# Kernel optimization log

Hardware: AMD Instinct MI355X
Metric: run time of the kernel (lower is better)

## Reference

```python
import jax, jax.numpy as jnp
import numpy as np
from jax import lax

THRESH = 0.6      # pnet score threshold (threshold[0])
IOU_THR = 0.5     # per-scale nms threshold in detect_face
K_PICKS = 128     # fixed max number of NMS picks (jit-static)
STRIDE = 2.0
CELL = 12.0
NEG = -1e30


def _conv(x, w, b):
    y = lax.conv_general_dilated(x, w, (1, 1), 'VALID',
                                 dimension_numbers=('NCHW', 'OIHW', 'NCHW'))
    return y + b[None, :, None, None]


def _prelu(x, a):
    return jnp.where(x > 0, x, a[None, :, None, None] * x)


def _maxpool2(x):
    return lax.reduce_window(x, -jnp.inf, lax.max, (1, 1, 2, 2), (1, 1, 2, 2), 'VALID')


def _nms(boxes, scores):
    # Greedy union-IoU NMS (nms_numpy math), vectorized with a fixed pick budget.
    # boxes [N,4] (shared grid), scores [N] with invalid entries already = NEG.
    x1, y1, x2, y2 = boxes[:, 0], boxes[:, 1], boxes[:, 2], boxes[:, 3]
    area = (x2 - x1 + 1.0) * (y2 - y1 + 1.0)

    def body(live, _):
        j = jnp.argmax(live)
        s = live[j]
        ok = s > NEG * 0.5
        xx1 = jnp.maximum(x1[j], x1); yy1 = jnp.maximum(y1[j], y1)
        xx2 = jnp.minimum(x2[j], x2); yy2 = jnp.minimum(y2[j], y2)
        inter = jnp.maximum(0.0, xx2 - xx1 + 1.0) * jnp.maximum(0.0, yy2 - yy1 + 1.0)
        iou = inter / (area[j] + area - inter)
        live = jnp.where(iou > IOU_THR, NEG, live).at[j].set(NEG)
        return live, (j, ok)

    _, (idx, ok) = lax.scan(body, scores, None, length=K_PICKS)
    return idx, ok


def setup_inputs():
    key = jax.random.key(0)
    ks = jax.random.split(key, 16)
    B, H, W = 16, 384, 512
    f = lambda k, shp, s=0.1: jax.random.normal(k, shp, jnp.float32) * s
    return {
        'im_data': jax.random.uniform(ks[0], (B, 3, H, W), jnp.float32) * 255.0,
        'c1_w': f(ks[1], (10, 3, 3, 3)), 'c1_b': f(ks[2], (10,)),
        'p1': jnp.full((10,), 0.25, jnp.float32),
        'c2_w': f(ks[3], (16, 10, 3, 3)), 'c2_b': f(ks[4], (16,)),
        'p2': jnp.full((16,), 0.25, jnp.float32),
        'c3_w': f(ks[5], (32, 16, 3, 3)), 'c3_b': f(ks[6], (32,)),
        'p3': jnp.full((32,), 0.25, jnp.float32),
        'c41_w': f(ks[7], (2, 32, 1, 1)), 'c41_b': f(ks[8], (2,)),
        'c42_w': f(ks[9], (4, 32, 1, 1)), 'c42_b': f(ks[10], (4,)),
    }


def reference(im_data, c1_w, c1_b, p1, c2_w, c2_b, p2, c3_w, c3_b, p3,
              c41_w, c41_b, c42_w, c42_b):
    # --- PNet conv trunk (detect_face normalization + MTCNN PNet) ---
    x = (im_data - 127.5) * 0.0078125
    h = _prelu(_conv(x, c1_w, c1_b), p1)
    h = _maxpool2(h)                                   # 2x2 s2 (dims even -> ceil==floor)
    h = _prelu(_conv(h, c2_w, c2_b), p2)
    h = _prelu(_conv(h, c3_w, c3_b), p3)
    probs = jax.nn.softmax(_conv(h, c41_w, c41_b), axis=1)[:, 1]   # [B,Hp,Wp]
    reg = _conv(h, c42_w, c42_b)                                   # [B,4,Hp,Wp]

    # --- generateBoundingBox (dense, masked instead of nonzero; scale=1) ---
    B, Hp, Wp = probs.shape
    yy, xx = jnp.meshgrid(jnp.arange(Hp, dtype=jnp.float32),
                          jnp.arange(Wp, dtype=jnp.float32), indexing='ij')
    boxes4 = jnp.stack([jnp.floor(STRIDE * xx + 1.0).ravel(),
                        jnp.floor(STRIDE * yy + 1.0).ravel(),
                        jnp.floor(STRIDE * xx + CELL).ravel(),
                        jnp.floor(STRIDE * yy + CELL).ravel()], axis=1)  # [N,4]
    scores = probs.reshape(B, -1)                                   # [B,N]
    regf = reg.reshape(B, 4, -1).transpose(0, 2, 1)                 # [B,N,4]
    masked = jnp.where(scores >= THRESH, scores, NEG)

    # --- per-image greedy NMS (batched_nms: images independent) ---
    idx, ok = jax.vmap(_nms, in_axes=(None, 0))(boxes4, masked)     # [B,K]
    pb = boxes4[idx]                                                # [B,K,4]
    ps = jnp.take_along_axis(scores, idx, axis=1)                   # [B,K]
    pr = jnp.take_along_axis(regf, idx[..., None], axis=1)          # [B,K,4]

    w = pb[..., 2] - pb[..., 0]
    hh = pb[..., 3] - pb[..., 1]
    q1 = pb[..., 0] + pr[..., 0] * w
    q2 = pb[..., 1] + pr[..., 1] * hh
    q3 = pb[..., 2] + pr[..., 2] * w
    q4 = pb[..., 3] + pr[..., 3] * hh
    rw = q3 - q1
    rh = q4 - q2
    l = jnp.maximum(rw, rh)
    nx1 = q1 + rw * 0.5 - l * 0.5
    ny1 = q2 + rh * 0.5 - l * 0.5
    out = jnp.stack([nx1, ny1, nx1 + l, ny1 + l, ps], axis=-1)      # [B,K,5]
    return out * ok[..., None].astype(out.dtype)
```

## Files before the change

kernel.cpp:

```cpp
#include <hip/hip_runtime.h>
#include <math.h>

#define BATCH 16
#define IH 384
#define IW 512
#define C1 10
#define P1H 191
#define P1W 255
#define P1S 256
#define C2 16
#define H2 189
#define W2 253
#define C3 32
#define H3 187
#define W3 251
#define N3 (H3*W3)
#define KP 128
#define CAP 7680
#define NEGV (-1e30f)

typedef _Float16 f16x8 __attribute__((ext_vector_type(8)));
typedef _Float16 f16x4 __attribute__((ext_vector_type(4)));
typedef float    f32x16 __attribute__((ext_vector_type(16)));

#define PXT 66
#define NSUB 2

#define T1R 34
#define T1C 68
__global__ __launch_bounds__(256, 1) void k_conv1pool(
        const float* __restrict__ im, const float* __restrict__ w,
        const float* __restrict__ bia, const float* __restrict__ slope,
        float* __restrict__ outp,
        const float* __restrict__ w3, _Float16* __restrict__ wbuf) {
    __shared__ float T[3 * T1R * T1C];

    int tx = threadIdx.x, ty = threadIdx.y;
    int tid = ty * 16 + tx;
    int bx = blockIdx.x, by = blockIdx.y, bb = blockIdx.z;

    if (bx == 0 && by == 0 && bb == 0) {
        for (int e = tid; e < 4608; e += 256) {
            int oc = e / 144;
            int rem = e - oc * 144;
            int ic = rem / 9;
            int tap = rem - ic * 9;
            float v = w3[e];
            _Float16 h = (_Float16)v;
            _Float16 l = (_Float16)(v - (float)h);
            int d = ((tap * 2 + (ic >> 3)) * 32 + oc) * 8 + (ic & 7);
            wbuf[d] = h;
            wbuf[4608 + d] = l;
        }
    }

    const size_t ibase = (size_t)bb * 3 * IH * IW;
    for (int g = tid; g < 3 * T1R * 33; g += 256) {
        int ch = g / (T1R * 33);
        int rem = g - ch * (T1R * 33);
        int r = rem / 33;
        int c2 = rem - r * 33;
        int yg = 32 * by + r;
        int xg = 64 * bx + 2 * c2;
        float2 v = make_float2(0.f, 0.f);
        if (yg < IH && xg < IW)
            v = *(const float2*)(im + ibase + ((size_t)ch * IH + yg) * IW + xg);
        float2 o;
        o.x = (v.x - 127.5f) * 0.0078125f;
        o.y = (v.y - 127.5f) * 0.0078125f;
        *(float2*)&T[(ch * T1R + r) * T1C + 2 * c2] = o;
    }
    __syncthreads();

    int Y  = by * 16 + ty;
    int X0 = bx * 32 + 2 * tx;
    if (Y >= P1H) return;

    float win[3][4][6];
    #pragma unroll
    for (int ch = 0; ch < 3; ++ch)
        #pragma unroll
        for (int r = 0; r < 4; ++r) {
            const float* p = &T[(ch * T1R + 2 * ty + r) * T1C + 4 * tx];
            float4 a = *(const float4*)p;
            float2 b = *(const float2*)(p + 4);
            win[ch][r][0] = a.x; win[ch][r][1] = a.y;
            win[ch][r][2] = a.z; win[ch][r][3] = a.w;
            win[ch][r][4] = b.x; win[ch][r][5] = b.y;
        }
    #pragma unroll
    for (int ch = 0; ch < 3; ++ch)
        #pragma unroll
        for (int r = 0; r < 4; ++r)
            #pragma unroll
            for (int c = 0; c < 6; ++c)
                asm volatile("" : "+v"(win[ch][r][c]));

    bool px1ok = (X0 + 1 < P1W);
    for (int oc = 0; oc < C1; ++oc) {
        const float* wo = w + oc * 27;
        float bv = bia[oc], sv = slope[oc];
        float c0 = bv, c1 = bv, c2 = bv, c3 = bv;
        float c4 = bv, c5 = bv, c6 = bv, c7 = bv;
        #pragma unroll
        for (int ch = 0; ch < 3; ++ch)
            #pragma unroll
            for (int ky = 0; ky < 3; ++ky)
                #pragma unroll
                for (int kx = 0; kx < 3; ++kx) {
                    float wv = wo[(ch * 3 + ky) * 3 + kx];
                    c0 += win[ch][0 + ky][0 + kx] * wv;
                    c1 += win[ch][0 + ky][1 + kx] * wv;
                    c2 += win[ch][0 + ky][2 + kx] * wv;
                    c3 += win[ch][0 + ky][3 + kx] * wv;
                    c4 += win[ch][1 + ky][0 + kx] * wv;
                    c5 += win[ch][1 + ky][1 + kx] * wv;
                    c6 += win[ch][1 + ky][2 + kx] * wv;
                    c7 += win[ch][1 + ky][3 + kx] * wv;
                }
        float m0 = fmaxf(fmaxf(c0, c1), fmaxf(c4, c5));
        float m1 = fmaxf(fmaxf(c2, c3), fmaxf(c6, c7));
        float p0 = m0 > 0.f ? m0 : sv * m0;
        float p1 = m1 > 0.f ? m1 : sv * m1;
        float* o = outp + (((size_t)bb * C1 + oc) * P1H + Y) * P1S + X0;
        o[0] = p0;
        if (px1ok) o[1] = p1;
    }
}

__global__ __launch_bounds__(256, 2) void k_conv2(
        const float* __restrict__ inp, const float* __restrict__ w,
        const float* __restrict__ bia, const float* __restrict__ slope,
        float* __restrict__ outp) {
    int x0 = (blockIdx.x * 64 + threadIdx.x) * 2;
    int y  = blockIdx.y * 4 + threadIdx.y;
    int bb = blockIdx.z;
    if (x0 >= W2 || y >= H2) return;

    float a0[C2], a1[C2];
    #pragma unroll
    for (int oc = 0; oc < C2; ++oc) { a0[oc] = bia[oc]; a1[oc] = bia[oc]; }

    bool tail = (x0 + 3 > P1W - 1);

    for (int ci = 0; ci < C1; ++ci) {
        const float* p = inp + (((size_t)bb * C1 + ci) * P1H + y) * P1S + x0;
        float v[3][4];
        #pragma unroll
        for (int r = 0; r < 3; ++r) {
            const float* pr = p + (size_t)r * P1S;
            float2 u0 = *(const float2*)pr;
            float2 u1 = *(const float2*)(pr + 2);
            v[r][0] = u0.x; v[r][1] = u0.y; v[r][2] = u1.x;
            v[r][3] = tail ? 0.f : u1.y;
        }
        const float* wc = w + ci * 9;
        #pragma unroll
        for (int oc = 0; oc < C2; ++oc) {
            const float* wo = wc + oc * (C1 * 9);
            float s0 = a0[oc], s1 = a1[oc];
            #pragma unroll
            for (int ky = 0; ky < 3; ++ky)
                #pragma unroll
                for (int kx = 0; kx < 3; ++kx) {
                    float wv = wo[ky * 3 + kx];
                    s0 += v[ky][kx]     * wv;
                    s1 += v[ky][kx + 1] * wv;
                }
            a0[oc] = s0; a1[oc] = s1;
        }
    }
    #pragma unroll
    for (int oc = 0; oc < C2; ++oc) {
        float sl = slope[oc];
        float u0 = a0[oc]; a0[oc] = u0 > 0.f ? u0 : sl * u0;
        float u1 = a1[oc]; a1[oc] = u1 > 0.f ? u1 : sl * u1;
    }
    float* o = outp + (((size_t)bb * H2 + y) * W2 + x0) * C2;
    float4* o4 = (float4*)o;
    o4[0] = make_float4(a0[0],  a0[1],  a0[2],  a0[3]);
    o4[1] = make_float4(a0[4],  a0[5],  a0[6],  a0[7]);
    o4[2] = make_float4(a0[8],  a0[9],  a0[10], a0[11]);
    o4[3] = make_float4(a0[12], a0[13], a0[14], a0[15]);
    if (x0 + 1 < W2) {
        float4* p4 = (float4*)(o + C2);
        p4[0] = make_float4(a1[0],  a1[1],  a1[2],  a1[3]);
        p4[1] = make_float4(a1[4],  a1[5],  a1[6],  a1[7]);
        p4[2] = make_float4(a1[8],  a1[9],  a1[10], a1[11]);
        p4[3] = make_float4(a1[12], a1[13], a1[14], a1[15]);
    }
}

__global__ __launch_bounds__(256, 2) void k_conv3mfma(
        const float* __restrict__ act,
        const _Float16* __restrict__ wbuf,
        const float* __restrict__ b3, const float* __restrict__ s3,
        const float* __restrict__ w41, const float* __restrict__ b41,
        const float* __restrict__ w42, const float* __restrict__ b42,
        float* __restrict__ scores, float4* __restrict__ regf) {
    __shared__ __align__(16) _Float16 Ah[6 * 2 * PXT * 8];
    __shared__ __align__(16) _Float16 Al[6 * 2 * PXT * 8];
    __shared__ __align__(16) float    htab[32 * 8];

    int tid = threadIdx.x;
    int bx = blockIdx.x * (NSUB * 32);
    int by = blockIdx.y * 4;
    int bb = blockIdx.z;

    {
        int oc = tid >> 3, f = tid & 7;
        float v;
        if      (f == 0) v = b3[oc];
        else if (f == 1) v = s3[oc];
        else if (f == 2) v = w41[oc];
        else if (f == 3) v = w41[32 + oc];
        else             v = w42[(f - 4) * 32 + oc];
        htab[tid] = v;
    }
    {
        const float* actb = act + (size_t)bb * H2 * W2 * C2;
        for (int e = tid; e < 6 * PXT * 4; e += 256) {
            int ic4 = e & 3;
            int t = e >> 2;
            int px = t % PXT;
            int row = t / PXT;
            int yg = by + row, xg = bx + px;
            float4 v = make_float4(0.f, 0.f, 0.f, 0.f);
            if (yg < H2 && xg < W2)
                v = *(const float4*)(actb + ((size_t)yg * W2 + xg) * C2 + ic4 * 4);
            float xs0 = v.x, xs1 = v.y, xs2 = v.z, xs3 = v.w;
            f16x4 hv, lv;
            _Float16 h;
            h = (_Float16)xs0; hv[0] = h; lv[0] = (_Float16)(xs0 - (float)h);
            h = (_Float16)xs1; hv[1] = h; lv[1] = (_Float16)(xs1 - (float)h);
            h = (_Float16)xs2; hv[2] = h; lv[2] = (_Float16)(xs2 - (float)h);
            h = (_Float16)xs3; hv[3] = h; lv[3] = (_Float16)(xs3 - (float)h);
            int kg = ic4 >> 1, h4 = ic4 & 1;
            int gr = (row * 2 + kg) * PXT + px;
            *(f16x4*)(Ah + gr * 8 + h4 * 4) = hv;
            *(f16x4*)(Al + gr * 8 + h4 * 4) = lv;
        }
    }
    __syncthreads();

    int wv = tid >> 6, lane = tid & 63;
    int col = lane & 31, half = lane >> 5;
    int y = by + wv;
    if (y >= H3) return;

    f32x16 acc[NSUB];
    #pragma unroll
    for (int s = 0; s < NSUB; ++s)
        #pragma unroll
        for (int i = 0; i < 16; ++i) acc[s][i] = 0.f;

    const _Float16* wg = wbuf + (half * 32 + col) * 8;

    #pragma unroll 1
    for (int ky = 0; ky < 3; ++ky) {
        const _Float16* arh = Ah + ((wv + ky) * 2 + half) * (PXT * 8);
        const _Float16* arl = Al + ((wv + ky) * 2 + half) * (PXT * 8);
        #pragma unroll
        for (int kx = 0; kx < 3; ++kx) {
            int tap = ky * 3 + kx;
            f16x8 wh = *(const f16x8*)(wg + tap * 512);
            f16x8 wl = *(const f16x8*)(wg + 4608 + tap * 512);
            #pragma unroll
            for (int s = 0; s < NSUB; ++s) {
                int p = s * 32 + col + kx;
                f16x8 bh = *(const f16x8*)(arh + p * 8);
                f16x8 bl = *(const f16x8*)(arl + p * 8);
                acc[s] = __builtin_amdgcn_mfma_f32_32x32x16_f16(wh, bh, acc[s], 0, 0, 0);
                acc[s] = __builtin_amdgcn_mfma_f32_32x32x16_f16(wl, bh, acc[s], 0, 0, 0);
                acc[s] = __builtin_amdgcn_mfma_f32_32x32x16_f16(wh, bl, acc[s], 0, 0, 0);
            }
        }
    }

    float L0[NSUB], L1[NSUB], R0[NSUB], R1[NSUB], R2[NSUB], R3[NSUB];
    #pragma unroll
    for (int s = 0; s < NSUB; ++s) { L0[s]=0.f; L1[s]=0.f; R0[s]=0.f; R1[s]=0.f; R2[s]=0.f; R3[s]=0.f; }

    #pragma unroll
    for (int r = 0; r < 16; ++r) {
        int oc = (r & 3) + 8 * (r >> 2) + 4 * half;
        float4 t0 = *(const float4*)&htab[oc * 8];
        float4 t1 = *(const float4*)&htab[oc * 8 + 4];
        #pragma unroll
        for (int s = 0; s < NSUB; ++s) {
            float v = acc[s][r] + t0.x;
            v = v > 0.f ? v : v * t0.y;
            L0[s] += v * t0.z; L1[s] += v * t0.w;
            R0[s] += v * t1.x; R1[s] += v * t1.y;
            R2[s] += v * t1.z; R3[s] += v * t1.w;
        }
    }

    float hb0 = b41[0], hb1 = b41[1];
    float rb0 = b42[0], rb1 = b42[1], rb2 = b42[2], rb3 = b42[3];

    #pragma unroll
    for (int s = 0; s < NSUB; ++s) {
        float l0 = L0[s] + __shfl_xor(L0[s], 32) + hb0;
        float l1 = L1[s] + __shfl_xor(L1[s], 32) + hb1;
        float r0 = R0[s] + __shfl_xor(R0[s], 32) + rb0;
        float r1 = R1[s] + __shfl_xor(R1[s], 32) + rb1;
        float r2 = R2[s] + __shfl_xor(R2[s], 32) + rb2;
        float r3 = R3[s] + __shfl_xor(R3[s], 32) + rb3;
        float m = fmaxf(l0, l1);
        float e0 = expf(l0 - m), e1 = expf(l1 - m);
        float p = e1 / (e0 + e1);
        int px = bx + s * 32 + col;
        if (half == 0 && px < W3) {
            size_t n = (size_t)bb * N3 + (size_t)y * W3 + px;
            scores[n] = (p >= 0.6f) ? p : NEGV;
            regf[n] = make_float4(r0, r1, r2, r3);
        }
    }
}

__global__ __launch_bounds__(512) void k_nms(
        const float* __restrict__ scores, const float4* __restrict__ regf,
        float* __restrict__ outp) {
    __shared__ float s_score[CAP];
    __shared__ int   s_idx[CAP];
    __shared__ float r_s[2][8];
    __shared__ int   r_i[2][8];
    __shared__ float s_picks[KP];
    __shared__ int   s_picki[KP];
    __shared__ int   s_misc[4];

    int tid = threadIdx.x;
    int bb = blockIdx.x;
    const float* sc = scores + (size_t)bb * N3;

    if (tid < 4) s_misc[tid] = 0;
    __syncthreads();

    int cnt = 0;
    for (int i = tid; i < N3; i += 512) if (sc[i] > 0.f) cnt++;
    atomicAdd(&s_misc[0], cnt);
    __syncthreads();
    int M = s_misc[0];

    int cutbin = 0;
    if (M > CAP) {
        for (int i = tid; i < 2048; i += 512) s_idx[i] = 0;
        __syncthreads();
        for (int i = tid; i < N3; i += 512) {
            float s = sc[i];
            if (s > 0.f) {
                int b = (int)((s - 0.6f) * 5120.f);
                b = b < 0 ? 0 : (b > 2047 ? 2047 : b);
                atomicAdd(&s_idx[b], 1);
            }
        }
        __syncthreads();
        if (tid == 0) {
            int accum = 0, b = 2047;
            for (; b >= 0; --b) {
                int c = s_idx[b];
                if (accum + c > CAP) break;
                accum += c;
            }
            s_misc[2] = b + 1;
        }
        __syncthreads();
        cutbin = s_misc[2];
        __syncthreads();
    }

    for (int i = tid; i < N3; i += 512) {
        float s = sc[i];
        if (s > 0.f) {
            bool keep = true;
            if (M > CAP) {
                int b = (int)((s - 0.6f) * 5120.f);
                b = b < 0 ? 0 : (b > 2047 ? 2047 : b);
                keep = (b >= cutbin);
            }
            if (keep) {
                int pos = atomicAdd(&s_misc[1], 1);
                if (pos < CAP) { s_score[pos] = s; s_idx[pos] = i; }
            }
        }
    }
    __syncthreads();
    int M2 = s_misc[1]; if (M2 > CAP) M2 = CAP;

    int np = 0;
    int   ppi = -1;
    float px1 = 0.f, py1 = 0.f, px2 = 0.f, py2 = 0.f;
    for (int pick = 0; pick < KP; ++pick) {
        float bs = -INFINITY; int bi = 0x7fffffff;
        for (int i = tid; i < M2; i += 512) {
            float s = s_score[i];
            if (ppi >= 0 && s > NEGV * 0.5f) {
                int id = s_idx[i];
                int cx = id % W3, cy = id / W3;
                float x1 = (float)(2 * cx + 1), y1 = (float)(2 * cy + 1);
                float x2 = (float)(2 * cx + 12), y2 = (float)(2 * cy + 12);
                float xx1 = fmaxf(px1, x1), yy1 = fmaxf(py1, y1);
                float xx2 = fminf(px2, x2), yy2 = fminf(py2, y2);
                float inter = fmaxf(0.f, xx2 - xx1 + 1.f) * fmaxf(0.f, yy2 - yy1 + 1.f);
                float iou = inter / (288.f - inter);
                if (iou > 0.5f) { s = NEGV; s_score[i] = NEGV; }
            }
            int id = s_idx[i];
            if (s > bs || (s == bs && id < bi)) { bs = s; bi = id; }
        }
        #pragma unroll
        for (int off = 32; off; off >>= 1) {
            float os = __shfl_down(bs, off);
            int   oi = __shfl_down(bi, off);
            if (os > bs || (os == bs && oi < bi)) { bs = os; bi = oi; }
        }
        int lane = tid & 63, wv = tid >> 6, buf = pick & 1;
        if (lane == 0) { r_s[buf][wv] = bs; r_i[buf][wv] = bi; }
        __syncthreads();
        float ps = r_s[buf][0]; int pi = r_i[buf][0];
        #pragma unroll
        for (int k = 1; k < 8; ++k) {
            float os = r_s[buf][k]; int oi = r_i[buf][k];
            if (os > ps || (os == ps && oi < pi)) { ps = os; pi = oi; }
        }
        if (ps < 0.f) break;
        if (tid == 0) { s_picks[pick] = ps; s_picki[pick] = pi; }
        np = pick + 1;

        ppi = pi;
        int pcx = pi % W3, pcy = pi / W3;
        px1 = (float)(2 * pcx + 1);  py1 = (float)(2 * pcy + 1);
        px2 = (float)(2 * pcx + 12); py2 = (float)(2 * pcy + 12);
    }
    __syncthreads();

    if (tid < KP) {
        float* o = outp + ((size_t)bb * KP + tid) * 5;
        if (tid < np) {
            int pi = s_picki[tid]; float ps = s_picks[tid];
            int cx = pi % W3, cy = pi / W3;
            float x1 = (float)(2 * cx + 1), y1 = (float)(2 * cy + 1);
            float x2 = (float)(2 * cx + 12), y2 = (float)(2 * cy + 12);
            float4 r = regf[(size_t)bb * N3 + pi];
            float wd = x2 - x1, hh = y2 - y1;
            float q1 = x1 + r.x * wd, q2 = y1 + r.y * hh;
            float q3 = x2 + r.z * wd, q4 = y2 + r.w * hh;
            float rw = q3 - q1, rh = q4 - q2;
            float L = fmaxf(rw, rh);
            float nx1 = q1 + rw * 0.5f - L * 0.5f;
            float ny1 = q2 + rh * 0.5f - L * 0.5f;
            o[0] = nx1; o[1] = ny1; o[2] = nx1 + L; o[3] = ny1 + L; o[4] = ps;
        } else {
            o[0] = 0.f; o[1] = 0.f; o[2] = 0.f; o[3] = 0.f; o[4] = 0.f;
        }
    }
}

extern "C" void kernel_launch(void* const* d_in, const int* in_sizes, int n_in,
                              void* d_out, int out_size, void* d_ws, size_t ws_size,
                              hipStream_t stream) {
    const float* im   = (const float*)d_in[0];
    const float* c1w  = (const float*)d_in[1];
    const float* c1b  = (const float*)d_in[2];
    const float* p1   = (const float*)d_in[3];
    const float* c2w  = (const float*)d_in[4];
    const float* c2b  = (const float*)d_in[5];
    const float* p2   = (const float*)d_in[6];
    const float* c3w  = (const float*)d_in[7];
    const float* c3b  = (const float*)d_in[8];
    const float* p3   = (const float*)d_in[9];
    const float* c41w = (const float*)d_in[10];
    const float* c41b = (const float*)d_in[11];
    const float* c42w = (const float*)d_in[12];
    const float* c42b = (const float*)d_in[13];

    float* ws = (float*)d_ws;
    const size_t P1FLOATS = (size_t)BATCH * C1 * P1H * P1S;
    float*  pool1   = ws;
    float*  conv2b  = ws + P1FLOATS;
    float*  scoresb = ws;
    float4* regfb   = (float4*)(ws + (size_t)BATCH * N3);
    _Float16* wbuf = (_Float16*)d_out;

    k_conv1pool<<<dim3(8, 12, BATCH), dim3(16, 16), 0, stream>>>(im, c1w, c1b, p1, pool1,
                                                                 c3w, wbuf);
    k_conv2   <<<dim3(2, 48, BATCH), dim3(64, 4), 0, stream>>>(pool1, c2w, c2b, p2, conv2b);
    k_conv3mfma<<<dim3(4, 47, BATCH), dim3(256), 0, stream>>>(conv2b, wbuf, c3b, p3,
                                                              c41w, c41b, c42w, c42b,
                                                              scoresb, regfb);
    k_nms<<<dim3(BATCH), dim3(512), 0, stream>>>(scoresb, regfb, (float*)d_out);
}
```

Before: 244.0 us.

## Move conv2 onto fp16 split-precision MFMA with LDS-staged tiles

Replaces the scalar FMA conv2 kernel with an MFMA-based kernel that stages pool1 rows into shared memory as hi/lo fp16 pairs and computes three 32x32x16 MFMAs per tap to approximate fp32 precision. The conv2 weights are repacked, padded from 10 to 16 input channels and from 16 to 32 output channels, inside the conv1 kernel's first block. This targets the ALU-bound scalar convolution at the cost of wasted MFMA lanes from padding and a 3x MFMA count for the precision split. It also merges the conv1 pair store into a single float2 write.

```diff
diff --git a/kernel.cpp b/kernel.cpp
--- a/kernel.cpp
+++ b/kernel.cpp
@@ -24,6 +24,7 @@
 typedef float    f32x16 __attribute__((ext_vector_type(16)));
 
 #define PXT 66
+#define PXT2 68
 #define NSUB 2
 
 #define T1R 34
@@ -32,7 +33,8 @@
         const float* __restrict__ im, const float* __restrict__ w,
         const float* __restrict__ bia, const float* __restrict__ slope,
         float* __restrict__ outp,
-        const float* __restrict__ w3, _Float16* __restrict__ wbuf) {
+        const float* __restrict__ w3, const float* __restrict__ w2,
+        _Float16* __restrict__ wbuf, _Float16* __restrict__ wbuf2) {
     __shared__ float T[3 * T1R * T1C];
 
     int tx = threadIdx.x, ty = threadIdx.y;
@@ -51,6 +53,19 @@
             int d = ((tap * 2 + (ic >> 3)) * 32 + oc) * 8 + (ic & 7);
             wbuf[d] = h;
             wbuf[4608 + d] = l;
+        }
+        for (int e = tid; e < 4608; e += 256) {
+            int tap = e / 512;
+            int rem = e - tap * 512;
+            int half = rem >> 8;
+            int oc = (rem >> 3) & 31;
+            int j = e & 7;
+            int ic = half * 8 + j;
+            float v = 0.f;
+            if (oc < 16 && ic < 10) v = w2[(oc * 10 + ic) * 9 + tap];
+            _Float16 h = (_Float16)v;
+            wbuf2[e] = h;
+            wbuf2[4608 + e] = (_Float16)(v - (float)h);
         }
     }
 
@@ -123,71 +138,108 @@
         float p0 = m0 > 0.f ? m0 : sv * m0;
         float p1 = m1 > 0.f ? m1 : sv * m1;
         float* o = outp + (((size_t)bb * C1 + oc) * P1H + Y) * P1S + X0;
-        o[0] = p0;
-        if (px1ok) o[1] = p1;
+        if (px1ok) *(float2*)o = make_float2(p0, p1);
+        else       o[0] = p0;
     }
 }
 
-__global__ __launch_bounds__(256, 2) void k_conv2(
-        const float* __restrict__ inp, const float* __restrict__ w,
-        const float* __restrict__ bia, const float* __restrict__ slope,
+__global__ __launch_bounds__(256, 2) void k_conv2mfma(
+        const float* __restrict__ pool1,
+        const _Float16* __restrict__ wbuf2,
+        const float* __restrict__ b2, const float* __restrict__ s2,
         float* __restrict__ outp) {
-    int x0 = (blockIdx.x * 64 + threadIdx.x) * 2;
-    int y  = blockIdx.y * 4 + threadIdx.y;
+    __shared__ __align__(16) _Float16 Ah[6 * 2 * PXT2 * 8];
+    __shared__ __align__(16) _Float16 Al[6 * 2 * PXT2 * 8];
+    __shared__ float htab[32];
+
+    int tid = threadIdx.x;
+    int bx = blockIdx.x * 64;
+    int by = blockIdx.y * 4;
     int bb = blockIdx.z;
-    if (x0 >= W2 || y >= H2) return;
-
-    float a0[C2], a1[C2];
-    #pragma unroll
-    for (int oc = 0; oc < C2; ++oc) { a0[oc] = bia[oc]; a1[oc] = bia[oc]; }
-
-    bool tail = (x0 + 3 > P1W - 1);
-
-    for (int ci = 0; ci < C1; ++ci) {
-        const float* p = inp + (((size_t)bb * C1 + ci) * P1H + y) * P1S + x0;
-        float v[3][4];
-        #pragma unroll
-        for (int r = 0; r < 3; ++r) {
-            const float* pr = p + (size_t)r * P1S;
-            float2 u0 = *(const float2*)pr;
-            float2 u1 = *(const float2*)(pr + 2);
-            v[r][0] = u0.x; v[r][1] = u0.y; v[r][2] = u1.x;
-            v[r][3] = tail ? 0.f : u1.y;
-        }
-        const float* wc = w + ci * 9;
-        #pragma unroll
-        for (int oc = 0; oc < C2; ++oc) {
-            const float* wo = wc + oc * (C1 * 9);
-            float s0 = a0[oc], s1 = a1[oc];
+
+    if (tid < 32) htab[tid] = (tid < 16) ? b2[tid] : s2[tid - 16];
+
+    {
+        const float* pin = pool1 + (size_t)bb * C1 * P1H * P1S;
+        for (int e = tid; e < 6 * 16 * 17; e += 256) {
+            int row = e / (16 * 17);
+            int rem = e - row * (16 * 17);
+            int ic  = rem / 17;
+            int c4  = (rem - ic * 17) * 4;
+            int yg = by + row;
+            int xg = bx + c4;
+            float4 v = make_float4(0.f, 0.f, 0.f, 0.f);
+            if (ic < C1 && yg < P1H) {
+                const float* src = pin + ((size_t)ic * P1H + yg) * P1S + xg;
+                if (xg + 3 < P1W) v = *(const float4*)src;
+                else {
+                    if (xg     < P1W) v.x = src[0];
+                    if (xg + 1 < P1W) v.y = src[1];
+                    if (xg + 2 < P1W) v.z = src[2];
+                }
+            }
+            int kg = ic >> 3, j = ic & 7;
+            int base = ((row * 2 + kg) * PXT2 + c4) * 8 + j;
+            _Float16 h;
+            h = (_Float16)v.x; Ah[base]      = h; Al[base]      = (_Float16)(v.x - (float)h);
+            h = (_Float16)v.y; Ah[base + 8]  = h; Al[base + 8]  = (_Float16)(v.y - (float)h);
+            h = (_Float16)v.z; Ah[base + 16] = h; Al[base + 16] = (_Float16)(v.z - (float)h);
+            h = (_Float16)v.w; Ah[base + 24] = h; Al[base + 24] = (_Float16)(v.w - (float)h);
+        }
+    }
+    __syncthreads();
+
+    int wv = tid >> 6, lane = tid & 63;
+    int col = lane & 31, half = lane >> 5;
+    int y = by + wv;
+    if (y >= H2) return;
+
+    f32x16 acc[NSUB];
+    #pragma unroll
+    for (int s = 0; s < NSUB; ++s)
+        #pragma unroll
+        for (int i = 0; i < 16; ++i) acc[s][i] = 0.f;
+
+    const _Float16* wg = wbuf2 + (half * 32 + col) * 8;
+
+    #pragma unroll 1
+    for (int ky = 0; ky < 3; ++ky) {
+        const _Float16* arh = Ah + ((wv + ky) * 2 + half) * (PXT2 * 8);
+        const _Float16* arl = Al + ((wv + ky) * 2 + half) * (PXT2 * 8);
+        #pragma unroll
+        for (int kx = 0; kx < 3; ++kx) {
+            int tap = ky * 3 + kx;
+            f16x8 wh = *(const f16x8*)(wg + tap * 512);
+            f16x8 wl = *(const f16x8*)(wg + 4608 + tap * 512);
             #pragma unroll
-            for (int ky = 0; ky < 3; ++ky)
-                #pragma unroll
-                for (int kx = 0; kx < 3; ++kx) {
-                    float wv = wo[ky * 3 + kx];
-                    s0 += v[ky][kx]     * wv;
-                    s1 += v[ky][kx + 1] * wv;
-                }
-            a0[oc] = s0; a1[oc] = s1;
-        }
-    }
-    #pragma unroll
-    for (int oc = 0; oc < C2; ++oc) {
-        float sl = slope[oc];
-        float u0 = a0[oc]; a0[oc] = u0 > 0.f ? u0 : sl * u0;
-        float u1 = a1[oc]; a1[oc] = u1 > 0.f ? u1 : sl * u1;
-    }
-    float* o = outp + (((size_t)bb * H2 + y) * W2 + x0) * C2;
-    float4* o4 = (float4*)o;
-    o4[0] = make_float4(a0[0],  a0[1],  a0[2],  a0[3]);
-    o4[1] = make_float4(a0[4],  a0[5],  a0[6],  a0[7]);
-    o4[2] = make_float4(a0[8],  a0[9],  a0[10], a0[11]);
-    o4[3] = make_float4(a0[12], a0[13], a0[14], a0[15]);
-    if (x0 + 1 < W2) {
-        float4* p4 = (float4*)(o + C2);
-        p4[0] = make_float4(a1[0],  a1[1],  a1[2],  a1[3]);
-        p4[1] = make_float4(a1[4],  a1[5],  a1[6],  a1[7]);
-        p4[2] = make_float4(a1[8],  a1[9],  a1[10], a1[11]);
-        p4[3] = make_float4(a1[12], a1[13], a1[14], a1[15]);
+            for (int s = 0; s < NSUB; ++s) {
+                int p = s * 32 + col + kx;
+                f16x8 bh = *(const f16x8*)(arh + p * 8);
+                f16x8 bl = *(const f16x8*)(arl + p * 8);
+                acc[s] = __builtin_amdgcn_mfma_f32_32x32x16_f16(wh, bh, acc[s], 0, 0, 0);
+                acc[s] = __builtin_amdgcn_mfma_f32_32x32x16_f16(wl, bh, acc[s], 0, 0, 0);
+                acc[s] = __builtin_amdgcn_mfma_f32_32x32x16_f16(wh, bl, acc[s], 0, 0, 0);
+            }
+        }
+    }
+
+    int oc0 = 4 * half, oc1 = 8 + 4 * half;
+    #pragma unroll
+    for (int s = 0; s < NSUB; ++s) {
+        int px = bx + s * 32 + col;
+        if (px < W2) {
+            float q[8];
+            #pragma unroll
+            for (int r = 0; r < 8; ++r) {
+                int oc = (r < 4) ? (oc0 + r) : (oc1 + r - 4);
+                float v = acc[s][r] + htab[oc];
+                float sl = htab[16 + oc];
+                q[r] = v > 0.f ? v : sl * v;
+            }
+            float* o = outp + (((size_t)bb * H2 + y) * W2 + px) * C2;
+            *(float4*)(o + oc0) = make_float4(q[0], q[1], q[2], q[3]);
+            *(float4*)(o + oc1) = make_float4(q[4], q[5], q[6], q[7]);
+        }
     }
 }
 
@@ -481,11 +533,12 @@
     float*  conv2b  = ws + P1FLOATS;
     float*  scoresb = ws;
     float4* regfb   = (float4*)(ws + (size_t)BATCH * N3);
-    _Float16* wbuf = (_Float16*)d_out;
+    _Float16* wbuf  = (_Float16*)d_out;
+    _Float16* wbuf2 = wbuf + 9216;
 
     k_conv1pool<<<dim3(8, 12, BATCH), dim3(16, 16), 0, stream>>>(im, c1w, c1b, p1, pool1,
-                                                                 c3w, wbuf);
-    k_conv2   <<<dim3(2, 48, BATCH), dim3(64, 4), 0, stream>>>(pool1, c2w, c2b, p2, conv2b);
+                                                                 c3w, c2w, wbuf, wbuf2);
+    k_conv2mfma<<<dim3(4, 48, BATCH), dim3(256), 0, stream>>>(pool1, wbuf2, c2b, p2, conv2b);
     k_conv3mfma<<<dim3(4, 47, BATCH), dim3(256), 0, stream>>>(conv2b, wbuf, c3b, p3,
                                                               c41w, c41b, c42w, c42b,
                                                               scoresb, regfb);
```

Result: faster. 235.0 us (-3.7%).
